# Kernel tuning notes

Hardware: AMD Instinct MI355X
Metric: run time of the kernel (lower is better)

## Reference

```python
import jax, jax.numpy as jnp
import numpy as np

N_NODES = 100000


def gcn_conv(x, W, b, src, dst, n):
    # PyG GCNConv: add self-loops, symmetric deg^{-1/2} normalization,
    # h = x @ W, out[i] = sum_j norm_ij * h[j] + b
    loop = jnp.arange(n, dtype=src.dtype)
    s = jnp.concatenate([src, loop])
    d = jnp.concatenate([dst, loop])
    h = x @ W  # [N, F_out]
    deg = jax.ops.segment_sum(jnp.ones_like(d, dtype=x.dtype), d, num_segments=n)
    dinv = jnp.where(deg > 0, jax.lax.rsqrt(deg), 0.0)
    norm = dinv[s] * dinv[d]  # [E+N]
    msgs = h[s] * norm[:, None]  # gather + scale
    out = jax.ops.segment_sum(msgs, d, num_segments=n)  # scatter-add
    return out + b


def setup_inputs() -> dict:
    key = jax.random.key(0)
    ks = jax.random.split(key, 8)
    n, e = N_NODES, 1600000
    return {
        "clinical": jax.random.normal(ks[0], (n, 64), dtype=jnp.float32),
        "mel": jax.random.normal(ks[1], (n, 1024), dtype=jnp.float32),
        "edge_index": jax.random.randint(ks[2], (2, e), 0, n, dtype=jnp.int64),
        "W_mel": jax.random.normal(ks[3], (1024, 128), dtype=jnp.float32) * 0.03,
        "b_mel": jnp.zeros((128,), dtype=jnp.float32),
        "W_cat": jax.random.normal(ks[4], (192, 128), dtype=jnp.float32) * 0.07,
        "b_cat": jnp.zeros((128,), dtype=jnp.float32),
        "W1": jax.random.normal(ks[5], (128, 128), dtype=jnp.float32) * 0.09,
        "b1": jnp.zeros((128,), dtype=jnp.float32),
        "W2": jax.random.normal(ks[6], (128, 4), dtype=jnp.float32) * 0.09,
        "b2": jnp.zeros((4,), dtype=jnp.float32),
    }


def reference(clinical, mel, edge_index, W_mel, b_mel, W_cat, b_cat, W1, b1, W2, b2):
    n = clinical.shape[0]
    src, dst = edge_index[0], edge_index[1]
    m = jax.nn.relu(mel @ W_mel + b_mel)            # [N, 128]
    x = jnp.concatenate([clinical, m], axis=1)       # [N, 192]
    x = jax.nn.relu(x @ W_cat + b_cat)               # [N, 128]
    x = jax.nn.relu(gcn_conv(x, W1, b1, src, dst, n))
    x = gcn_conv(x, W2, b2, src, dst, n)             # [N, 4]
    return x
```

## Files before the change

### kernel.cpp

```cpp
#include <hip/hip_runtime.h>
#include <cstdint>


typedef short short4_t __attribute__((ext_vector_type(4)));
typedef short short8_t __attribute__((ext_vector_type(8)));
typedef float floatx4 __attribute__((ext_vector_type(4)));

__device__ __forceinline__ short f2bf(float f) {
  union { float f; unsigned u; } v;
  v.f = f;
  unsigned r = v.u + 0x7fffu + ((v.u >> 16) & 1u);
  return (short)(r >> 16);
}

__device__ __forceinline__ bool detect_i64(const int* __restrict__ ei) {
  int nz = 0;
#pragma unroll
  for (int i = 1; i < 64; i += 2) nz |= ei[i];
  return nz == 0;
}
__device__ __forceinline__ int load_src(const int* __restrict__ ei, int e, bool is64) {
  return is64 ? ei[2 * e] : ei[e];
}
__device__ __forceinline__ int load_dst(const int* __restrict__ ei, int e, int E, bool is64) {
  return is64 ? ei[2 * (E + e)] : ei[E + e];
}

__global__ __launch_bounds__(256) void zero_int_k(int* __restrict__ p, int n) {
  int i = blockIdx.x * 256 + threadIdx.x;
  if (i < n) p[i] = 0;
}

__global__ __launch_bounds__(256) void count_deg_k(const int* __restrict__ ei,
                                                   int* __restrict__ degi, int E) {
  const bool is64 = detect_i64(ei);
  int e = blockIdx.x * 256 + threadIdx.x;
  if (e < E) atomicAdd(&degi[load_dst(ei, e, E, is64)], 1);
}

__global__ __launch_bounds__(256) void dinv_k(const int* __restrict__ degi,
                                              float* __restrict__ dinv, int n) {
  int i = blockIdx.x * 256 + threadIdx.x;
  if (i < n) dinv[i] = rsqrtf((float)degi[i] + 1.0f);
}

__global__ __launch_bounds__(256) void scan_reduce_k(const int* __restrict__ degi,
                                                     int* __restrict__ partial, int n) {
  __shared__ int s[256];
  int t = threadIdx.x;
  int i = blockIdx.x * 256 + t;
  s[t] = (i < n) ? degi[i] : 0;
  __syncthreads();
#pragma unroll
  for (int off = 128; off > 0; off >>= 1) {
    if (t < off) s[t] += s[t + off];
    __syncthreads();
  }
  if (t == 0) partial[blockIdx.x] = s[0];
}

__global__ __launch_bounds__(512) void scan_partials_k(const int* __restrict__ partial,
                                                       int* __restrict__ excl, int B,
                                                       int* __restrict__ rowptr, int n, int E) {
  __shared__ int s[512];
  int t = threadIdx.x;
  int v = (t < B) ? partial[t] : 0;
  s[t] = v;
  __syncthreads();
  for (int off = 1; off < 512; off <<= 1) {
    int x = (t >= off) ? s[t - off] : 0;
    __syncthreads();
    s[t] += x;
    __syncthreads();
  }
  if (t < B) excl[t] = s[t] - v;
  if (t == 0) rowptr[n] = E;
}

__global__ __launch_bounds__(256) void scan_final_k(const int* __restrict__ degi,
                                                    const int* __restrict__ excl,
                                                    int* __restrict__ rowptr, int n) {
  __shared__ int s[256];
  int t = threadIdx.x;
  int i = blockIdx.x * 256 + t;
  int v = (i < n) ? degi[i] : 0;
  s[t] = v;
  __syncthreads();
  for (int off = 1; off < 256; off <<= 1) {
    int x = (t >= off) ? s[t - off] : 0;
    __syncthreads();
    s[t] += x;
    __syncthreads();
  }
  if (i < n) rowptr[i] = excl[blockIdx.x] + s[t] - v;
}

__global__ __launch_bounds__(256) void fill_col_k(const int* __restrict__ ei,
                                                  const int* __restrict__ rowptr,
                                                  int* __restrict__ fill,
                                                  int* __restrict__ col, int E) {
  const bool is64 = detect_i64(ei);
  int e = blockIdx.x * 256 + threadIdx.x;
  if (e < E) {
    int s = load_src(ei, e, is64);
    int d = load_dst(ei, e, E, is64);
    int pos = rowptr[d] + atomicAdd(&fill[d], 1);
    col[pos] = s;
  }
}

__global__ __launch_bounds__(256) void convW_k(const float* __restrict__ W,
                                               short* __restrict__ Wt) {
  int idx = blockIdx.x * 256 + threadIdx.x;
  int nn = idx >> 10;
  int k = idx & 1023;
  Wt[idx] = f2bf(W[(size_t)k * 128 + nn]);
}

__global__ __launch_bounds__(256) void mel_gemm_mfma_k(const float* __restrict__ A,
                                                       const short* __restrict__ Wt,
                                                       const float* __restrict__ bias,
                                                       float* __restrict__ C, int n) {
  const int tid = threadIdx.x;
  const int lane = tid & 63;
  const int wv = tid >> 6;
  const int quad = lane >> 4;
  const int cbase = lane & 15;
  const int row0 = blockIdx.x * 128;

  int r0 = row0 + wv * 32 + cbase;
  int r1 = r0 + 16;
  if (r0 > n - 1) r0 = n - 1;
  if (r1 > n - 1) r1 = n - 1;
  const float* __restrict__ a0p = A + (size_t)r0 * 1024;
  const float* __restrict__ a1p = A + (size_t)r1 * 1024;
  const short* __restrict__ bp = Wt + (size_t)cbase * 1024;

  floatx4 acc[2][8];
#pragma unroll
  for (int tr = 0; tr < 2; ++tr)
#pragma unroll
    for (int tc = 0; tc < 8; ++tc) acc[tr][tc] = (floatx4){0.f, 0.f, 0.f, 0.f};

  for (int kc = 0; kc < 16; ++kc) {
#pragma unroll
    for (int kk = 0; kk < 2; ++kk) {
      const int kb = kc * 64 + kk * 32 + quad * 8;
      floatx4 va00 = *(const floatx4*)(a0p + kb);
      floatx4 va01 = *(const floatx4*)(a0p + kb + 4);
      floatx4 va10 = *(const floatx4*)(a1p + kb);
      floatx4 va11 = *(const floatx4*)(a1p + kb + 4);
      short8_t af0, af1;
#pragma unroll
      for (int j = 0; j < 4; ++j) {
        af0[j] = f2bf(va00[j]);
        af0[j + 4] = f2bf(va01[j]);
        af1[j] = f2bf(va10[j]);
        af1[j + 4] = f2bf(va11[j]);
      }
#pragma unroll
      for (int tc = 0; tc < 8; ++tc) {
        short8_t bf = *(const short8_t*)(bp + (size_t)tc * 16384 + kb);
        acc[0][tc] = __builtin_amdgcn_mfma_f32_16x16x32_bf16(af0, bf, acc[0][tc], 0, 0, 0);
        acc[1][tc] = __builtin_amdgcn_mfma_f32_16x16x32_bf16(af1, bf, acc[1][tc], 0, 0, 0);
      }
    }
  }

  float bb[8];
#pragma unroll
  for (int tc = 0; tc < 8; ++tc) bb[tc] = bias[tc * 16 + cbase];
#pragma unroll
  for (int tr = 0; tr < 2; ++tr) {
#pragma unroll
    for (int r = 0; r < 4; ++r) {
      int grow = row0 + wv * 32 + tr * 16 + quad * 4 + r;
      if (grow < n) {
#pragma unroll
        for (int tc = 0; tc < 8; ++tc) {
          float v = acc[tr][tc][r] + bb[tc];
          C[(size_t)grow * 128 + tc * 16 + cbase] = fmaxf(v, 0.f);
        }
      }
    }
  }
}

template <bool RELU, bool HASBIAS>
__global__ __launch_bounds__(256) void gemm128_k(const float* __restrict__ A, int K,
                                                 const float* __restrict__ B,
                                                 const float* __restrict__ bias,
                                                 float* __restrict__ C, int n) {
  __shared__ float As[64][33];
  __shared__ float4 Bs[32][32];
  const int tid = threadIdx.x;
  const int tx = tid & 31, ty = tid >> 5;
  const int row0 = blockIdx.x * 64;
  float acc[8][4];
#pragma unroll
  for (int i = 0; i < 8; ++i)
#pragma unroll
    for (int j = 0; j < 4; ++j) acc[i][j] = 0.f;

  const int nChunks = K >> 5;
  for (int kc = 0; kc < nChunks; ++kc) {
    __syncthreads();
#pragma unroll
    for (int j = 0; j < 2; ++j) {
      int idx = tid + j * 256;
      int ar = idx >> 3, ac4 = idx & 7;
      int grow = row0 + ar;
      float4 v = make_float4(0.f, 0.f, 0.f, 0.f);
      if (grow < n) v = *(const float4*)(A + (size_t)grow * K + kc * 32 + ac4 * 4);
      As[ar][ac4 * 4 + 0] = v.x;
      As[ar][ac4 * 4 + 1] = v.y;
      As[ar][ac4 * 4 + 2] = v.z;
      As[ar][ac4 * 4 + 3] = v.w;
    }
#pragma unroll
    for (int j = 0; j < 4; ++j) {
      int idx = tid + j * 256;
      int br = idx >> 5, bc4 = idx & 31;
      Bs[br][bc4] = *(const float4*)(B + (size_t)(kc * 32 + br) * 128 + bc4 * 4);
    }
    __syncthreads();
#pragma unroll
    for (int kk = 0; kk < 32; ++kk) {
      float4 b = Bs[kk][tx];
#pragma unroll
      for (int i = 0; i < 8; ++i) {
        float a = As[ty * 8 + i][kk];
        acc[i][0] += a * b.x;
        acc[i][1] += a * b.y;
        acc[i][2] += a * b.z;
        acc[i][3] += a * b.w;
      }
    }
  }
  float4 bb = make_float4(0.f, 0.f, 0.f, 0.f);
  if (HASBIAS) bb = *(const float4*)(bias + tx * 4);
#pragma unroll
  for (int i = 0; i < 8; ++i) {
    int grow = row0 + ty * 8 + i;
    if (grow < n) {
      float4 o;
      o.x = acc[i][0] + bb.x;
      o.y = acc[i][1] + bb.y;
      o.z = acc[i][2] + bb.z;
      o.w = acc[i][3] + bb.w;
      if (RELU) {
        o.x = fmaxf(o.x, 0.f);
        o.y = fmaxf(o.y, 0.f);
        o.z = fmaxf(o.z, 0.f);
        o.w = fmaxf(o.w, 0.f);
      }
      *(float4*)(C + (size_t)grow * 128 + tx * 4) = o;
    }
  }
}

__global__ __launch_bounds__(256) void gemm_cat_k(const float* __restrict__ A1,
                                                  const float* __restrict__ A2,
                                                  const float* __restrict__ B,
                                                  const float* __restrict__ bias,
                                                  float* __restrict__ C, int n) {
  __shared__ float As[64][33];
  __shared__ float4 Bs[32][32];
  const int tid = threadIdx.x;
  const int tx = tid & 31, ty = tid >> 5;
  const int row0 = blockIdx.x * 64;
  float acc[8][4];
#pragma unroll
  for (int i = 0; i < 8; ++i)
#pragma unroll
    for (int j = 0; j < 4; ++j) acc[i][j] = 0.f;

  for (int kc = 0; kc < 6; ++kc) {
    __syncthreads();
#pragma unroll
    for (int j = 0; j < 2; ++j) {
      int idx = tid + j * 256;
      int ar = idx >> 3, ac4 = idx & 7;
      int grow = row0 + ar;
      int kcol = kc * 32 + ac4 * 4;
      float4 v = make_float4(0.f, 0.f, 0.f, 0.f);
      if (grow < n) {
        v = (kcol < 64) ? *(const float4*)(A1 + (size_t)grow * 64 + kcol)
                        : *(const float4*)(A2 + (size_t)grow * 128 + (kcol - 64));
      }
      As[ar][ac4 * 4 + 0] = v.x;
      As[ar][ac4 * 4 + 1] = v.y;
      As[ar][ac4 * 4 + 2] = v.z;
      As[ar][ac4 * 4 + 3] = v.w;
    }
#pragma unroll
    for (int j = 0; j < 4; ++j) {
      int idx = tid + j * 256;
      int br = idx >> 5, bc4 = idx & 31;
      Bs[br][bc4] = *(const float4*)(B + (size_t)(kc * 32 + br) * 128 + bc4 * 4);
    }
    __syncthreads();
#pragma unroll
    for (int kk = 0; kk < 32; ++kk) {
      float4 b = Bs[kk][tx];
#pragma unroll
      for (int i = 0; i < 8; ++i) {
        float a = As[ty * 8 + i][kk];
        acc[i][0] += a * b.x;
        acc[i][1] += a * b.y;
        acc[i][2] += a * b.z;
        acc[i][3] += a * b.w;
      }
    }
  }
  float4 bb = *(const float4*)(bias + tx * 4);
#pragma unroll
  for (int i = 0; i < 8; ++i) {
    int grow = row0 + ty * 8 + i;
    if (grow < n) {
      float4 o;
      o.x = fmaxf(acc[i][0] + bb.x, 0.f);
      o.y = fmaxf(acc[i][1] + bb.y, 0.f);
      o.z = fmaxf(acc[i][2] + bb.z, 0.f);
      o.w = fmaxf(acc[i][3] + bb.w, 0.f);
      *(float4*)(C + (size_t)grow * 128 + tx * 4) = o;
    }
  }
}

template <bool RELU>
__global__ __launch_bounds__(256) void gather128_k(const int* __restrict__ col,
                                                   const int* __restrict__ rowptr,
                                                   const float* __restrict__ dinv,
                                                   const float* __restrict__ h,
                                                   const float* __restrict__ bias,
                                                   float* __restrict__ out, int n) {
  const int node = blockIdx.x * 2 + (threadIdx.x >> 7);
  const int f = threadIdx.x & 127;
  if (node >= n) return;
  const int beg = rowptr[node], end = rowptr[node + 1];
  float acc = 0.f;
  int p = beg;
  for (; p + 4 <= end; p += 4) {
    int s0 = col[p], s1 = col[p + 1], s2 = col[p + 2], s3 = col[p + 3];
    float d0 = dinv[s0], d1 = dinv[s1], d2 = dinv[s2], d3 = dinv[s3];
    float h0 = h[(size_t)s0 * 128 + f];
    float h1 = h[(size_t)s1 * 128 + f];
    float h2 = h[(size_t)s2 * 128 + f];
    float h3 = h[(size_t)s3 * 128 + f];
    acc += d0 * h0 + d1 * h1 + d2 * h2 + d3 * h3;
  }
  for (; p < end; ++p) {
    int s = col[p];
    acc += dinv[s] * h[(size_t)s * 128 + f];
  }
  const float di = dinv[node];
  float v = di * (acc + di * h[(size_t)node * 128 + f]) + bias[f];
  if (RELU) v = fmaxf(v, 0.f);
  out[(size_t)node * 128 + f] = v;
}

__global__ __launch_bounds__(256) void gemm_small4_k(const float* __restrict__ A,
                                                     const float* __restrict__ W,
                                                     float* __restrict__ Y, int n) {
  __shared__ float Ws[512];
  int tid = threadIdx.x;
  Ws[tid] = W[tid];
  Ws[tid + 256] = W[tid + 256];
  __syncthreads();
  int row = blockIdx.x * 256 + tid;
  if (row >= n) return;
  const float4* A4 = (const float4*)(A + (size_t)row * 128);
  float a0 = 0.f, a1 = 0.f, a2 = 0.f, a3 = 0.f;
#pragma unroll
  for (int k4 = 0; k4 < 32; ++k4) {
    float4 a = A4[k4];
    const float* w = &Ws[k4 * 16];
    a0 += a.x * w[0] + a.y * w[4] + a.z * w[8] + a.w * w[12];
    a1 += a.x * w[1] + a.y * w[5] + a.z * w[9] + a.w * w[13];
    a2 += a.x * w[2] + a.y * w[6] + a.z * w[10] + a.w * w[14];
    a3 += a.x * w[3] + a.y * w[7] + a.z * w[11] + a.w * w[15];
  }
  *(float4*)(Y + (size_t)row * 4) = make_float4(a0, a1, a2, a3);
}

__global__ __launch_bounds__(256) void gather4_k(const int* __restrict__ col,
                                                 const int* __restrict__ rowptr,
                                                 const float* __restrict__ dinv,
                                                 const float* __restrict__ y,
                                                 const float* __restrict__ b2,
                                                 float* __restrict__ out, int n) {
  int node = blockIdx.x * 256 + threadIdx.x;
  if (node >= n) return;
  const int beg = rowptr[node], end = rowptr[node + 1];
  float ax = 0.f, ay = 0.f, az = 0.f, aw = 0.f;
  int p = beg;
  for (; p + 2 <= end; p += 2) {
    int s0 = col[p], s1 = col[p + 1];
    float d0 = dinv[s0], d1 = dinv[s1];
    float4 y0 = *(const float4*)(y + (size_t)s0 * 4);
    float4 y1 = *(const float4*)(y + (size_t)s1 * 4);
    ax += d0 * y0.x + d1 * y1.x;
    ay += d0 * y0.y + d1 * y1.y;
    az += d0 * y0.z + d1 * y1.z;
    aw += d0 * y0.w + d1 * y1.w;
  }
  for (; p < end; ++p) {
    int s = col[p];
    float ds = dinv[s];
    float4 yv = *(const float4*)(y + (size_t)s * 4);
    ax += ds * yv.x;
    ay += ds * yv.y;
    az += ds * yv.z;
    aw += ds * yv.w;
  }
  const float di = dinv[node];
  float4 yd = *(const float4*)(y + (size_t)node * 4);
  float4 o;
  o.x = di * (ax + di * yd.x) + b2[0];
  o.y = di * (ay + di * yd.y) + b2[1];
  o.z = di * (az + di * yd.z) + b2[2];
  o.w = di * (aw + di * yd.w) + b2[3];
  *(float4*)(out + (size_t)node * 4) = o;
}

extern "C" void kernel_launch(void* const* d_in, const int* in_sizes, int n_in,
                              void* d_out, int out_size, void* d_ws, size_t ws_size,
                              hipStream_t stream) {
  const float* clinical = (const float*)d_in[0];
  const float* mel = (const float*)d_in[1];
  const int* ei = (const int*)d_in[2];
  const float* W_mel = (const float*)d_in[3];
  const float* b_mel = (const float*)d_in[4];
  const float* W_cat = (const float*)d_in[5];
  const float* b_cat = (const float*)d_in[6];
  const float* W1 = (const float*)d_in[7];
  const float* b1 = (const float*)d_in[8];
  const float* W2 = (const float*)d_in[9];
  const float* b2 = (const float*)d_in[10];
  float* out = (float*)d_out;

  const int N = in_sizes[0] / 64;
  const int E = in_sizes[2] / 2;
  const int B = (N + 255) / 256;

  float* bufA = (float*)d_ws;
  float* bufB = bufA + (size_t)N * 128;
  float* dinv = bufB + (size_t)N * 128;
  float* ybuf = dinv + N;
  int* degi = (int*)(ybuf + (size_t)N * 4);
  int* rowptr = degi + N;
  int* fill = rowptr + (N + 1);
  int* partial = fill + N;
  int* excl = partial + 512;
  int* col = excl + 512;
  short* Wt = (short*)(col + E);

  const dim3 blk(256);

  zero_int_k<<<(N + 255) / 256, blk, 0, stream>>>(degi, N);
  count_deg_k<<<(E + 255) / 256, blk, 0, stream>>>(ei, degi, E);
  dinv_k<<<B, blk, 0, stream>>>(degi, dinv, N);
  scan_reduce_k<<<B, blk, 0, stream>>>(degi, partial, N);
  scan_partials_k<<<1, 512, 0, stream>>>(partial, excl, B, rowptr, N, E);
  scan_final_k<<<B, blk, 0, stream>>>(degi, excl, rowptr, N);
  zero_int_k<<<B, blk, 0, stream>>>(fill, N);
  fill_col_k<<<(E + 255) / 256, blk, 0, stream>>>(ei, rowptr, fill, col, E);
  convW_k<<<512, blk, 0, stream>>>(W_mel, Wt);

  mel_gemm_mfma_k<<<(N + 127) / 128, blk, 0, stream>>>(mel, Wt, b_mel, bufA, N);
  gemm_cat_k<<<(N + 63) / 64, blk, 0, stream>>>(clinical, bufA, W_cat, b_cat, bufB, N);
  gemm128_k<false, false><<<(N + 63) / 64, blk, 0, stream>>>(bufB, 128, W1, nullptr, bufA, N);

  gather128_k<true><<<(N + 1) / 2, blk, 0, stream>>>(col, rowptr, dinv, bufA, b1, bufB, N);

  gemm_small4_k<<<(N + 255) / 256, blk, 0, stream>>>(bufB, W2, ybuf, N);

  gather4_k<<<(N + 255) / 256, blk, 0, stream>>>(col, rowptr, dinv, ybuf, b2, out, N);
}
```

Baseline: 1.133 ms.

## Fuse concat GEMM and W1 GEMM into one split-bf16 MFMA kernel

Measured after the change: 1.099 ms. 1.03x faster.

```diff
diff --git a/kernel.cpp b/kernel.cpp
--- a/kernel.cpp
+++ b/kernel.cpp
@@ -11,6 +11,11 @@
   v.f = f;
   unsigned r = v.u + 0x7fffu + ((v.u >> 16) & 1u);
   return (short)(r >> 16);
+}
+__device__ __forceinline__ float bf2f(short h) {
+  union { unsigned u; float f; } v;
+  v.u = ((unsigned)(unsigned short)h) << 16;
+  return v.f;
 }
 
 __device__ __forceinline__ bool detect_i64(const int* __restrict__ ei) {
@@ -117,6 +122,18 @@
   Wt[idx] = f2bf(W[(size_t)k * 128 + nn]);
 }
 
+__global__ void convWsplit_k(const float* __restrict__ W, short* __restrict__ Thi,
+                             short* __restrict__ Tlo, int K) {
+  int c = blockIdx.x;
+  int k = threadIdx.x;
+  if (k >= K) return;
+  float w = W[(size_t)k * 128 + c];
+  short hi = f2bf(w);
+  short lo = f2bf(w - bf2f(hi));
+  Thi[(size_t)c * K + k] = hi;
+  Tlo[(size_t)c * K + k] = lo;
+}
+
 __global__ __launch_bounds__(256) void mel_gemm_mfma_k(const float* __restrict__ A,
                                                        const short* __restrict__ Wt,
                                                        const float* __restrict__ bias,
@@ -186,144 +203,136 @@
   }
 }
 
-template <bool RELU, bool HASBIAS>
-__global__ __launch_bounds__(256) void gemm128_k(const float* __restrict__ A, int K,
-                                                 const float* __restrict__ B,
-                                                 const float* __restrict__ bias,
-                                                 float* __restrict__ C, int n) {
-  __shared__ float As[64][33];
-  __shared__ float4 Bs[32][32];
+__global__ __launch_bounds__(256) void cat_w1_mfma_k(
+    const float* __restrict__ clin, const float* __restrict__ m,
+    const short* __restrict__ WcT_hi, const short* __restrict__ WcT_lo,
+    const short* __restrict__ W1T_hi, const short* __restrict__ W1T_lo,
+    const float* __restrict__ bcat, float* __restrict__ H, int n) {
+  __shared__ short Xhi[4][4096];
+  __shared__ short Xlo[4][4096];
   const int tid = threadIdx.x;
-  const int tx = tid & 31, ty = tid >> 5;
-  const int row0 = blockIdx.x * 64;
-  float acc[8][4];
-#pragma unroll
-  for (int i = 0; i < 8; ++i)
-#pragma unroll
-    for (int j = 0; j < 4; ++j) acc[i][j] = 0.f;
-
-  const int nChunks = K >> 5;
-  for (int kc = 0; kc < nChunks; ++kc) {
-    __syncthreads();
-#pragma unroll
-    for (int j = 0; j < 2; ++j) {
-      int idx = tid + j * 256;
-      int ar = idx >> 3, ac4 = idx & 7;
-      int grow = row0 + ar;
-      float4 v = make_float4(0.f, 0.f, 0.f, 0.f);
-      if (grow < n) v = *(const float4*)(A + (size_t)grow * K + kc * 32 + ac4 * 4);
-      As[ar][ac4 * 4 + 0] = v.x;
-      As[ar][ac4 * 4 + 1] = v.y;
-      As[ar][ac4 * 4 + 2] = v.z;
-      As[ar][ac4 * 4 + 3] = v.w;
-    }
+  const int lane = tid & 63;
+  const int wv = tid >> 6;
+  const int quad = lane >> 4;
+  const int cbase = lane & 15;
+  const int row0 = blockIdx.x * 128;
+
+  int r0 = row0 + wv * 32 + cbase;
+  int r1 = r0 + 16;
+  if (r0 > n - 1) r0 = n - 1;
+  if (r1 > n - 1) r1 = n - 1;
+  const float* __restrict__ c0p = clin + (size_t)r0 * 64;
+  const float* __restrict__ c1p = clin + (size_t)r1 * 64;
+  const float* __restrict__ m0p = m + (size_t)r0 * 128;
+  const float* __restrict__ m1p = m + (size_t)r1 * 128;
+
+  floatx4 acc[2][8];
+#pragma unroll
+  for (int tr = 0; tr < 2; ++tr)
+#pragma unroll
+    for (int tc = 0; tc < 8; ++tc) acc[tr][tc] = (floatx4){0.f, 0.f, 0.f, 0.f};
+
+#pragma unroll
+  for (int kb = 0; kb < 192; kb += 32) {
+    const int ko = kb + quad * 8;
+    floatx4 v0a, v0b, v1a, v1b;
+    if (kb < 64) {
+      v0a = *(const floatx4*)(c0p + ko);
+      v0b = *(const floatx4*)(c0p + ko + 4);
+      v1a = *(const floatx4*)(c1p + ko);
+      v1b = *(const floatx4*)(c1p + ko + 4);
+    } else {
+      v0a = *(const floatx4*)(m0p + ko - 64);
+      v0b = *(const floatx4*)(m0p + ko - 60);
+      v1a = *(const floatx4*)(m1p + ko - 64);
+      v1b = *(const floatx4*)(m1p + ko - 60);
+    }
+    short8_t a0h, a0l, a1h, a1l;
 #pragma unroll
     for (int j = 0; j < 4; ++j) {
-      int idx = tid + j * 256;
-      int br = idx >> 5, bc4 = idx & 31;
-      Bs[br][bc4] = *(const float4*)(B + (size_t)(kc * 32 + br) * 128 + bc4 * 4);
-    }
-    __syncthreads();
-#pragma unroll
-    for (int kk = 0; kk < 32; ++kk) {
-      float4 b = Bs[kk][tx];
-#pragma unroll
-      for (int i = 0; i < 8; ++i) {
-        float a = As[ty * 8 + i][kk];
-        acc[i][0] += a * b.x;
-        acc[i][1] += a * b.y;
-        acc[i][2] += a * b.z;
-        acc[i][3] += a * b.w;
-      }
-    }
-  }
-  float4 bb = make_float4(0.f, 0.f, 0.f, 0.f);
-  if (HASBIAS) bb = *(const float4*)(bias + tx * 4);
-#pragma unroll
-  for (int i = 0; i < 8; ++i) {
-    int grow = row0 + ty * 8 + i;
-    if (grow < n) {
-      float4 o;
-      o.x = acc[i][0] + bb.x;
-      o.y = acc[i][1] + bb.y;
-      o.z = acc[i][2] + bb.z;
-      o.w = acc[i][3] + bb.w;
-      if (RELU) {
-        o.x = fmaxf(o.x, 0.f);
-        o.y = fmaxf(o.y, 0.f);
-        o.z = fmaxf(o.z, 0.f);
-        o.w = fmaxf(o.w, 0.f);
-      }
-      *(float4*)(C + (size_t)grow * 128 + tx * 4) = o;
-    }
-  }
-}
-
-__global__ __launch_bounds__(256) void gemm_cat_k(const float* __restrict__ A1,
-                                                  const float* __restrict__ A2,
-                                                  const float* __restrict__ B,
-                                                  const float* __restrict__ bias,
-                                                  float* __restrict__ C, int n) {
-  __shared__ float As[64][33];
-  __shared__ float4 Bs[32][32];
-  const int tid = threadIdx.x;
-  const int tx = tid & 31, ty = tid >> 5;
-  const int row0 = blockIdx.x * 64;
-  float acc[8][4];
-#pragma unroll
-  for (int i = 0; i < 8; ++i)
-#pragma unroll
-    for (int j = 0; j < 4; ++j) acc[i][j] = 0.f;
-
-  for (int kc = 0; kc < 6; ++kc) {
-    __syncthreads();
-#pragma unroll
-    for (int j = 0; j < 2; ++j) {
-      int idx = tid + j * 256;
-      int ar = idx >> 3, ac4 = idx & 7;
-      int grow = row0 + ar;
-      int kcol = kc * 32 + ac4 * 4;
-      float4 v = make_float4(0.f, 0.f, 0.f, 0.f);
+      a0h[j] = f2bf(v0a[j]);     a0l[j] = f2bf(v0a[j] - bf2f(a0h[j]));
+      a0h[j + 4] = f2bf(v0b[j]); a0l[j + 4] = f2bf(v0b[j] - bf2f(a0h[j + 4]));
+      a1h[j] = f2bf(v1a[j]);     a1l[j] = f2bf(v1a[j] - bf2f(a1h[j]));
+      a1h[j + 4] = f2bf(v1b[j]); a1l[j + 4] = f2bf(v1b[j] - bf2f(a1h[j + 4]));
+    }
+#pragma unroll
+    for (int tc = 0; tc < 8; ++tc) {
+      const short* bpp = WcT_hi + (size_t)(tc * 16 + cbase) * 192 + ko;
+      const short* bpl = WcT_lo + (size_t)(tc * 16 + cbase) * 192 + ko;
+      short8_t bh = *(const short8_t*)bpp;
+      short8_t bl = *(const short8_t*)bpl;
+      acc[0][tc] = __builtin_amdgcn_mfma_f32_16x16x32_bf16(a0h, bh, acc[0][tc], 0, 0, 0);
+      acc[0][tc] = __builtin_amdgcn_mfma_f32_16x16x32_bf16(a0h, bl, acc[0][tc], 0, 0, 0);
+      acc[0][tc] = __builtin_amdgcn_mfma_f32_16x16x32_bf16(a0l, bh, acc[0][tc], 0, 0, 0);
+      acc[1][tc] = __builtin_amdgcn_mfma_f32_16x16x32_bf16(a1h, bh, acc[1][tc], 0, 0, 0);
+      acc[1][tc] = __builtin_amdgcn_mfma_f32_16x16x32_bf16(a1h, bl, acc[1][tc], 0, 0, 0);
+      acc[1][tc] = __builtin_amdgcn_mfma_f32_16x16x32_bf16(a1l, bh, acc[1][tc], 0, 0, 0);
+    }
+  }
+
+  float bb[8];
+#pragma unroll
+  for (int tc = 0; tc < 8; ++tc) bb[tc] = bcat[tc * 16 + cbase];
+  short* __restrict__ xh = &Xhi[wv][0];
+  short* __restrict__ xl = &Xlo[wv][0];
+#pragma unroll
+  for (int tr = 0; tr < 2; ++tr) {
+#pragma unroll
+    for (int tc = 0; tc < 8; ++tc) {
+      const int col = tc * 16 + cbase;
+#pragma unroll
+      for (int r = 0; r < 4; ++r) {
+        const int lrow = tr * 16 + quad * 4 + r;
+        float v = fmaxf(acc[tr][tc][r] + bb[tc], 0.f);
+        short hi = f2bf(v);
+        short lo = f2bf(v - bf2f(hi));
+        const int idx = (lrow * 128 + col) ^ ((lrow & 7) << 3);
+        xh[idx] = hi;
+        xl[idx] = lo;
+      }
+    }
+  }
+
+  floatx4 acc2[2][8];
+#pragma unroll
+  for (int tr = 0; tr < 2; ++tr)
+#pragma unroll
+    for (int tc = 0; tc < 8; ++tc) acc2[tr][tc] = (floatx4){0.f, 0.f, 0.f, 0.f};
+
+#pragma unroll
+  for (int kb = 0; kb < 128; kb += 32) {
+    const int k = kb + quad * 8;
+    short8_t ah[2], al[2];
+#pragma unroll
+    for (int tr = 0; tr < 2; ++tr) {
+      const int lrow = tr * 16 + cbase;
+      const int idx = (lrow * 128 + k) ^ ((lrow & 7) << 3);
+      ah[tr] = *(const short8_t*)&xh[idx];
+      al[tr] = *(const short8_t*)&xl[idx];
+    }
+#pragma unroll
+    for (int tc = 0; tc < 8; ++tc) {
+      short8_t bh = *(const short8_t*)(W1T_hi + (size_t)(tc * 16 + cbase) * 128 + k);
+      short8_t bl = *(const short8_t*)(W1T_lo + (size_t)(tc * 16 + cbase) * 128 + k);
+#pragma unroll
+      for (int tr = 0; tr < 2; ++tr) {
+        acc2[tr][tc] = __builtin_amdgcn_mfma_f32_16x16x32_bf16(ah[tr], bh, acc2[tr][tc], 0, 0, 0);
+        acc2[tr][tc] = __builtin_amdgcn_mfma_f32_16x16x32_bf16(ah[tr], bl, acc2[tr][tc], 0, 0, 0);
+        acc2[tr][tc] = __builtin_amdgcn_mfma_f32_16x16x32_bf16(al[tr], bh, acc2[tr][tc], 0, 0, 0);
+      }
+    }
+  }
+
+#pragma unroll
+  for (int tr = 0; tr < 2; ++tr) {
+#pragma unroll
+    for (int r = 0; r < 4; ++r) {
+      int grow = row0 + wv * 32 + tr * 16 + quad * 4 + r;
       if (grow < n) {
-        v = (kcol < 64) ? *(const float4*)(A1 + (size_t)grow * 64 + kcol)
-                        : *(const float4*)(A2 + (size_t)grow * 128 + (kcol - 64));
-      }
-      As[ar][ac4 * 4 + 0] = v.x;
-      As[ar][ac4 * 4 + 1] = v.y;
-      As[ar][ac4 * 4 + 2] = v.z;
-      As[ar][ac4 * 4 + 3] = v.w;
-    }
-#pragma unroll
-    for (int j = 0; j < 4; ++j) {
-      int idx = tid + j * 256;
-      int br = idx >> 5, bc4 = idx & 31;
-      Bs[br][bc4] = *(const float4*)(B + (size_t)(kc * 32 + br) * 128 + bc4 * 4);
-    }
-    __syncthreads();
-#pragma unroll
-    for (int kk = 0; kk < 32; ++kk) {
-      float4 b = Bs[kk][tx];
-#pragma unroll
-      for (int i = 0; i < 8; ++i) {
-        float a = As[ty * 8 + i][kk];
-        acc[i][0] += a * b.x;
-        acc[i][1] += a * b.y;
-        acc[i][2] += a * b.z;
-        acc[i][3] += a * b.w;
-      }
-    }
-  }
-  float4 bb = *(const float4*)(bias + tx * 4);
-#pragma unroll
-  for (int i = 0; i < 8; ++i) {
-    int grow = row0 + ty * 8 + i;
-    if (grow < n) {
-      float4 o;
-      o.x = fmaxf(acc[i][0] + bb.x, 0.f);
-      o.y = fmaxf(acc[i][1] + bb.y, 0.f);
-      o.z = fmaxf(acc[i][2] + bb.z, 0.f);
-      o.w = fmaxf(acc[i][3] + bb.w, 0.f);
-      *(float4*)(C + (size_t)grow * 128 + tx * 4) = o;
+#pragma unroll
+        for (int tc = 0; tc < 8; ++tc)
+          H[(size_t)grow * 128 + tc * 16 + cbase] = acc2[tr][tc][r];
+      }
     }
   }
 }
@@ -455,6 +464,10 @@
   int* excl = partial + 512;
   int* col = excl + 512;
   short* Wt = (short*)(col + E);
+  short* WcT_hi = Wt + 128 * 1024;
+  short* WcT_lo = WcT_hi + 128 * 192;
+  short* W1T_hi = WcT_lo + 128 * 192;
+  short* W1T_lo = W1T_hi + 128 * 128;
 
   const dim3 blk(256);
 
@@ -467,10 +480,12 @@
   zero_int_k<<<B, blk, 0, stream>>>(fill, N);
   fill_col_k<<<(E + 255) / 256, blk, 0, stream>>>(ei, rowptr, fill, col, E);
   convW_k<<<512, blk, 0, stream>>>(W_mel, Wt);
+  convWsplit_k<<<128, 192, 0, stream>>>(W_cat, WcT_hi, WcT_lo, 192);
+  convWsplit_k<<<128, 128, 0, stream>>>(W1, W1T_hi, W1T_lo, 128);
 
   mel_gemm_mfma_k<<<(N + 127) / 128, blk, 0, stream>>>(mel, Wt, b_mel, bufA, N);
-  gemm_cat_k<<<(N + 63) / 64, blk, 0, stream>>>(clinical, bufA, W_cat, b_cat, bufB, N);
-  gemm128_k<false, false><<<(N + 63) / 64, blk, 0, stream>>>(bufB, 128, W1, nullptr, bufA, N);
+  cat_w1_mfma_k<<<(N + 127) / 128, blk, 0, stream>>>(clinical, bufA, WcT_hi, WcT_lo,
+                                                     W1T_hi, W1T_lo, b_cat, bufA, N);
 
   gather128_k<true><<<(N + 1) / 2, blk, 0, stream>>>(col, rowptr, dinv, bufA, b1, bufB, N);
 
```
